# Kernel tuning notes

Hardware: AMD Instinct MI355X
Metric: run time of the kernel (lower is better)

Reference implementation:

```python
import jax, jax.numpy as jnp
import numpy as np

N = 100_000            # particles
E = 3_200_000          # edges (avg degree 32)
DIM = 3
H = 1.0                # kernel_radius
SIGMA = 3.0 / 359.0 / np.pi / H**3   # 3D quintic kernel normalization
RHO_REF = 1.0
P_REF = 100.0          # rho_ref * (10*u_ref)**2 / gamma, gamma=1
P_BG = 0.0             # p_bg_factor * p_ref
ETA0 = 0.01            # base_viscosity
EPS = 1e-8


def _qpows(d, p):
    q = d / H
    return (jnp.maximum(0.0, 1.0 - q) ** p,
            jnp.maximum(0.0, 2.0 - q) ** p,
            jnp.maximum(0.0, 3.0 - q) ** p)


def kernel_w(d):
    q1, q2, q3 = _qpows(d, 5)
    return SIGMA * (q3 - 6.0 * q2 + 15.0 * q1)


def kernel_grad_w(d):
    q1, q2, q3 = _qpows(d, 4)
    return (SIGMA / H) * (-5.0 * q3 + 30.0 * q2 - 75.0 * q1)


def setup_inputs() -> dict:
    key = jax.random.key(0)
    k1, k2, k3, k4 = jax.random.split(key, 4)
    r = jax.random.uniform(k1, (N, DIM), dtype=jnp.float32)   # positions in unit box
    v = jax.random.normal(k2, (N, DIM), dtype=jnp.float32)    # velocity history (last frame)
    i_s = jax.random.randint(k3, (E,), 0, N)                  # receivers
    j_s = jax.random.randint(k4, (E,), 0, N)                  # senders
    return {"r": r, "v": v, "i_s": i_s, "j_s": j_s}


def reference(r, v, i_s, j_s):
    n = r.shape[0]
    # --- per-edge gather + kernel ---
    dr = r[i_s] - r[j_s]                       # displacement_fn, [E,3]
    d = jnp.sqrt(jnp.sum(dr * dr, axis=-1))    # [E]
    w = kernel_w(d)
    # --- density summation (scatter) ---
    mass = jnp.ones((n,), r.dtype)
    rho = mass * jax.ops.segment_sum(w, i_s, num_segments=n)
    # Tait EoS, gamma=1
    p = P_REF * (rho / RHO_REF - 1.0) + P_BG
    eta = jnp.full((n,), ETA0, r.dtype)

    # --- per-edge acceleration (gather particle fields to edges) ---
    rho_i, rho_j = rho[i_s], rho[j_s]
    p_i, p_j = p[i_s], p[j_s]
    eta_i, eta_j = eta[i_s], eta[j_s]
    u_i, u_j = v[i_s], v[j_s]                  # u == v in _transform
    v_i, v_j = u_i, u_j

    eta_ij = 2.0 * eta_i * eta_j / (eta_i + eta_j + EPS)
    p_ij = (rho_j * p_i + rho_i * p_j) / (rho_i + rho_j)
    # ((m_i/rho_i)^2 + (m_j/rho_j)^2)/m_i with m == 1
    wvol = (1.0 / rho_i) ** 2 + (1.0 / rho_j) ** 2
    c = wvol * kernel_grad_w(d) / (d + EPS)    # [E]

    # transport stress A = (outer(rho_i*u_i, v_i-u_i) + outer(rho_j*u_j, v_j-u_j))/2, [E,3,3]
    A = 0.5 * (rho_i[:, None, None] * u_i[:, :, None] * (v_i - u_i)[:, None, :]
               + rho_j[:, None, None] * u_j[:, :, None] * (v_j - u_j)[:, None, :])
    Ar = jnp.einsum('eij,ej->ei', A, dr)

    a_eq_8 = c[:, None] * (-p_ij[:, None] * dr + Ar + eta_ij[:, None] * (u_i - u_j))
    p_bg_i = jnp.zeros_like(p_i)               # _transform passes zeros
    a_eq_13 = (c * p_bg_i)[:, None] * dr

    # --- scatter-reduce to particles ---
    dudt = jax.ops.segment_sum(a_eq_8, i_s, num_segments=n)   # [N,3]
    dvdt = jax.ops.segment_sum(a_eq_13, i_s, num_segments=n)  # [N,3]

    # pack state outputs: [rho, p, dudt(3), dvdt(3)] -> [N,8]
    return jnp.concatenate([rho[:, None], p[:, None], dudt, dvdt], axis=1)
```

## Files before the change

kernel.cpp:

```cpp
#include <hip/hip_runtime.h>
#include <math.h>

#ifndef M_PI
#define M_PI 3.14159265358979323846
#endif

static constexpr float kSigma = (float)(3.0 / 359.0 / M_PI);
static constexpr float kPRef  = 100.0f;
static constexpr float kEps   = 1e-8f;
static constexpr float kEta   = (float)(2.0 * 0.01 * 0.01 / (0.01 + 0.01 + 1e-8));

#define CHUNKA 8192

__device__ __forceinline__ float pow5f(float t) { float t2 = t * t; return t2 * t2 * t; }
__device__ __forceinline__ float pow4f(float t) { float t2 = t * t; return t2 * t2; }

__global__ void k_pack(const float* __restrict__ r, float4* __restrict__ pos4, int n) {
    int i = blockIdx.x * blockDim.x + threadIdx.x;
    if (i >= n) return;
    pos4[i] = make_float4(r[3 * i], r[3 * i + 1], r[3 * i + 2], 0.f);
}

__global__ void k_hist(const int* __restrict__ i_s, int* __restrict__ ghist,
                       int nbA, int nbins, int E, int shift) {
    __shared__ int h[512];
    int t = threadIdx.x, blk = blockIdx.x;
    for (int b = t; b < nbins; b += 512) h[b] = 0;
    __syncthreads();
    int base = blk * CHUNKA;
    int end = min(base + CHUNKA, E);
    for (int k = base + t; k < end; k += 512)
        atomicAdd(&h[i_s[k] >> shift], 1);
    __syncthreads();
    for (int b = t; b < nbins; b += 512)
        ghist[b * nbA + blk] = h[b];
}

__global__ void k_scan_block(const int* __restrict__ in, int* __restrict__ out,
                             int* __restrict__ bsum, int m) {
    __shared__ int s[256];
    int t = threadIdx.x;
    int i = blockIdx.x * 256 + t;
    int x = (i < m) ? in[i] : 0;
    s[t] = x;
    __syncthreads();
    for (int d = 1; d < 256; d <<= 1) {
        int v = (t >= d) ? s[t - d] : 0;
        __syncthreads();
        s[t] += v;
        __syncthreads();
    }
    if (i < m) out[i] = s[t] - x;
    if (t == 255) bsum[blockIdx.x] = s[255];
}

__global__ void k_scan_bsums(const int* __restrict__ bsum, int* __restrict__ bscan, int nb) {
    __shared__ int s[512];
    __shared__ int carry;
    int t = threadIdx.x;
    if (t == 0) carry = 0;
    __syncthreads();
    for (int base = 0; base < nb; base += 512) {
        int i = base + t;
        int x = (i < nb) ? bsum[i] : 0;
        s[t] = x;
        __syncthreads();
        for (int d = 1; d < 512; d <<= 1) {
            int v = (t >= d) ? s[t - d] : 0;
            __syncthreads();
            s[t] += v;
            __syncthreads();
        }
        if (i < nb) bscan[i] = s[t] - x + carry;
        __syncthreads();
        if (t == 511) carry += s[511];
        __syncthreads();
    }
}

__global__ void k_split(const int* __restrict__ i_s, const int* __restrict__ j_s,
                        const int* __restrict__ gscan, const int* __restrict__ bscan,
                        int* __restrict__ pairs, int nbA, int nbins, int E,
                        int shift, int jbits) {
    __shared__ int cur[512];
    int t = threadIdx.x, blk = blockIdx.x;
    for (int b = t; b < nbins; b += 512) {
        int idx = b * nbA + blk;
        cur[b] = gscan[idx] + bscan[idx >> 8];
    }
    __syncthreads();
    int fmask = (1 << shift) - 1;
    int base = blk * CHUNKA;
    int end = min(base + CHUNKA, E);
    for (int k = base + t; k < end; k += 512) {
        int i = i_s[k];
        int pos = atomicAdd(&cur[i >> shift], 1);
        pairs[pos] = ((i & fmask) << jbits) | j_s[k];
    }
}

__global__ void k_rho_bin(const float4* __restrict__ pos4, const float* __restrict__ v,
                          const int* __restrict__ pairs, const int* __restrict__ gscan,
                          const int* __restrict__ bscan, float4* __restrict__ pv8,
                          float* __restrict__ out, int nbA, int n, int E,
                          int shift, int jbits, int m) {
    __shared__ float srho[512];
    __shared__ float4 spos[512];
    __shared__ int sse[2];
    int b = blockIdx.x, t = threadIdx.x;
    int slots = 1 << shift;
    int lo = b << shift;
    for (int s0 = t; s0 < slots; s0 += 1024) {
        srho[s0] = 0.f;
        int i = lo + s0;
        spos[s0] = (i < n) ? pos4[i] : make_float4(0.f, 0.f, 0.f, 0.f);
    }
    if (t == 0) {
        int i0 = b * nbA;
        sse[0] = gscan[i0] + bscan[i0 >> 8];
        int i1 = (b + 1) * nbA;
        sse[1] = (i1 < m) ? (gscan[i1] + bscan[i1 >> 8]) : E;
    }
    __syncthreads();
    int s = sse[0], e = sse[1];
    int jm = (1 << jbits) - 1;
    for (int k = s + t; k < e; k += 1024) {
        int pr = pairs[k];
        int slot = pr >> jbits, j = pr & jm;
        float4 rj = pos4[j];
        float4 ri = spos[slot];
        float dx = ri.x - rj.x, dy = ri.y - rj.y, dz = ri.z - rj.z;
        float d = sqrtf(dx * dx + dy * dy + dz * dz);
        float t1 = fmaxf(1.f - d, 0.f);
        float t2 = fmaxf(2.f - d, 0.f);
        float t3 = fmaxf(3.f - d, 0.f);
        float w = kSigma * (pow5f(t3) - 6.f * pow5f(t2) + 15.f * pow5f(t1));
        atomicAdd(&srho[slot], w);
    }
    __syncthreads();
    for (int s0 = t; s0 < slots; s0 += 1024) {
        int i = lo + s0;
        if (i >= n) continue;
        float rh = srho[s0];
        float pp = kPRef * (rh - 1.0f);
        float4 sp = spos[s0];
        pv8[2 * i]     = make_float4(sp.x, sp.y, sp.z, rh);
        pv8[2 * i + 1] = make_float4(v[3 * i], v[3 * i + 1], v[3 * i + 2], pp);
        float* o = out + (size_t)i * 8;
        o[0] = rh;
        o[1] = pp;
        o[5] = 0.f; o[6] = 0.f; o[7] = 0.f;
    }
}

__global__ void k_acc_bin(const float4* __restrict__ pv8, const int* __restrict__ pairs,
                          const int* __restrict__ gscan, const int* __restrict__ bscan,
                          float* __restrict__ out, int nbA, int n, int E,
                          int shift, int jbits, int m) {
    __shared__ float sax[512], say[512], saz[512];
    __shared__ float4 sab[1024];
    __shared__ int sse[2];
    int b = blockIdx.x, t = threadIdx.x;
    int slots = 1 << shift;
    int lo = b << shift;
    for (int s0 = t; s0 < slots; s0 += 1024) { sax[s0] = 0.f; say[s0] = 0.f; saz[s0] = 0.f; }
    for (int q = t; q < 2 * slots; q += 1024) {
        int gi = 2 * lo + q;
        sab[q] = (gi < 2 * n) ? pv8[gi] : make_float4(0.f, 0.f, 0.f, 0.f);
    }
    if (t == 0) {
        int i0 = b * nbA;
        sse[0] = gscan[i0] + bscan[i0 >> 8];
        int i1 = (b + 1) * nbA;
        sse[1] = (i1 < m) ? (gscan[i1] + bscan[i1 >> 8]) : E;
    }
    __syncthreads();
    int s = sse[0], e = sse[1];
    int jm = (1 << jbits) - 1;
    for (int k = s + t; k < e; k += 1024) {
        int pr = pairs[k];
        int slot = pr >> jbits, j = pr & jm;
        float4 aj = pv8[2 * j];
        float4 bj = pv8[2 * j + 1];
        float4 ai = sab[2 * slot];
        float4 bi = sab[2 * slot + 1];
        float rho_i = ai.w, p_i = bi.w;
        float rho_j = aj.w, p_j = bj.w;
        float dx = ai.x - aj.x, dy = ai.y - aj.y, dz = ai.z - aj.z;
        float d = sqrtf(dx * dx + dy * dy + dz * dz);
        float t1 = fmaxf(1.f - d, 0.f);
        float t2 = fmaxf(2.f - d, 0.f);
        float t3 = fmaxf(3.f - d, 0.f);
        float gw = kSigma * (-5.f * pow4f(t3) + 30.f * pow4f(t2) - 75.f * pow4f(t1));
        float inv_i = 1.0f / rho_i, inv_j = 1.0f / rho_j;
        float c = (inv_i * inv_i + inv_j * inv_j) * gw / (d + kEps);
        float p_ij = (rho_j * p_i + rho_i * p_j) / (rho_i + rho_j);
        atomicAdd(&sax[slot], c * (kEta * (bi.x - bj.x) - p_ij * dx));
        atomicAdd(&say[slot], c * (kEta * (bi.y - bj.y) - p_ij * dy));
        atomicAdd(&saz[slot], c * (kEta * (bi.z - bj.z) - p_ij * dz));
    }
    __syncthreads();
    for (int s0 = t; s0 < slots; s0 += 1024) {
        int i = lo + s0;
        if (i >= n) continue;
        float* o = out + (size_t)i * 8 + 2;
        o[0] = sax[s0]; o[1] = say[s0]; o[2] = saz[s0];
    }
}

static inline char* wcarve(char*& ws, size_t bytes) {
    char* p = ws;
    ws += (bytes + 255) & ~(size_t)255;
    return p;
}

extern "C" void kernel_launch(void* const* d_in, const int* in_sizes, int n_in,
                              void* d_out, int out_size, void* d_ws, size_t ws_size,
                              hipStream_t stream) {
    const float* r = (const float*)d_in[0];
    const float* v = (const float*)d_in[1];
    const int* i_s = (const int*)d_in[2];
    const int* j_s = (const int*)d_in[3];
    int n = in_sizes[0] / 3;
    int E = in_sizes[2];
    float* out = (float*)d_out;

    int shift = 8;
    int nbins = ((n - 1) >> shift) + 1;
    while (nbins > 512) { shift++; nbins = ((n - 1) >> shift) + 1; }
    int jbits = 1;
    while ((1 << jbits) < n) jbits++;

    int nbA = (E + CHUNKA - 1) / CHUNKA;
    int m = nbins * nbA;
    int nb2 = (m + 255) / 256;

    char* ws = (char*)d_ws;
    float4* pos4  = (float4*)wcarve(ws, (size_t)n * 16);
    float4* pv8   = (float4*)wcarve(ws, (size_t)n * 32);
    int*    ghist = (int*)wcarve(ws, (size_t)m * 4);
    int*    gscan = (int*)wcarve(ws, (size_t)m * 4);
    int*    bsum  = (int*)wcarve(ws, (size_t)nb2 * 4);
    int*    bscan = (int*)wcarve(ws, (size_t)nb2 * 4);
    int*    pairs = (int*)wcarve(ws, (size_t)E * 4);

    const int bs = 256;
    int gn = (n + bs - 1) / bs;

    k_pack<<<gn, bs, 0, stream>>>(r, pos4, n);
    k_hist<<<nbA, 512, 0, stream>>>(i_s, ghist, nbA, nbins, E, shift);
    k_scan_block<<<nb2, 256, 0, stream>>>(ghist, gscan, bsum, m);
    k_scan_bsums<<<1, 512, 0, stream>>>(bsum, bscan, nb2);
    k_split<<<nbA, 512, 0, stream>>>(i_s, j_s, gscan, bscan, pairs, nbA, nbins, E, shift, jbits);
    k_rho_bin<<<nbins, 1024, 0, stream>>>(pos4, v, pairs, gscan, bscan, pv8, out, nbA, n, E, shift, jbits, m);
    k_acc_bin<<<nbins, 1024, 0, stream>>>(pv8, pairs, gscan, bscan, out, nbA, n, E, shift, jbits, m);
}
```

Measured before the change: 214.5 us.

## Split each bin's edges across eight sub-blocks with partial-sum reduction kernels

The per-bin density and acceleration kernels were one 1024-thread block per 256-particle bin (~391 blocks). Now each bin is split into eight sub-blocks of 256 threads, each handling a contiguous slice of the bin's edges. Each sub-block writes its shared-memory partial sums to global buffers, and new reduction kernels combine them and write the outputs. The histogram uses half-size chunks so the split kernel can index the finer scan at every other column. This raises block count and occupancy and cuts shared-atomic contention, at the cost of extra partial-buffer traffic and two extra launches.

Measured after the change: 210.9 us. No clear change (-1.6%).

```diff
diff --git a/kernel.cpp b/kernel.cpp
--- a/kernel.cpp
+++ b/kernel.cpp
@@ -10,7 +10,9 @@
 static constexpr float kEps   = 1e-8f;
 static constexpr float kEta   = (float)(2.0 * 0.01 * 0.01 / (0.01 + 0.01 + 1e-8));
 
-#define CHUNKA 8192
+#define CHUNKH 4096
+#define CHUNKS 8192
+#define NSUB   8
 
 __device__ __forceinline__ float pow5f(float t) { float t2 = t * t; return t2 * t2 * t; }
 __device__ __forceinline__ float pow4f(float t) { float t2 = t * t; return t2 * t2; }
@@ -22,18 +24,18 @@
 }
 
 __global__ void k_hist(const int* __restrict__ i_s, int* __restrict__ ghist,
-                       int nbA, int nbins, int E, int shift) {
+                       int nbAh, int nbins, int E, int shift) {
     __shared__ int h[512];
     int t = threadIdx.x, blk = blockIdx.x;
-    for (int b = t; b < nbins; b += 512) h[b] = 0;
-    __syncthreads();
-    int base = blk * CHUNKA;
-    int end = min(base + CHUNKA, E);
-    for (int k = base + t; k < end; k += 512)
+    for (int b = t; b < nbins; b += 256) h[b] = 0;
+    __syncthreads();
+    int base = blk * CHUNKH;
+    int end = min(base + CHUNKH, E);
+    for (int k = base + t; k < end; k += 256)
         atomicAdd(&h[i_s[k] >> shift], 1);
     __syncthreads();
-    for (int b = t; b < nbins; b += 512)
-        ghist[b * nbA + blk] = h[b];
+    for (int b = t; b < nbins; b += 256)
+        ghist[b * nbAh + blk] = h[b];
 }
 
 __global__ void k_scan_block(const int* __restrict__ in, int* __restrict__ out,
@@ -78,20 +80,23 @@
     }
 }
 
+__device__ __forceinline__ int scanned(const int* __restrict__ gscan,
+                                       const int* __restrict__ bscan, int idx) {
+    return gscan[idx] + bscan[idx >> 8];
+}
+
 __global__ void k_split(const int* __restrict__ i_s, const int* __restrict__ j_s,
                         const int* __restrict__ gscan, const int* __restrict__ bscan,
-                        int* __restrict__ pairs, int nbA, int nbins, int E,
+                        int* __restrict__ pairs, int nbAh, int nbins, int E,
                         int shift, int jbits) {
     __shared__ int cur[512];
     int t = threadIdx.x, blk = blockIdx.x;
-    for (int b = t; b < nbins; b += 512) {
-        int idx = b * nbA + blk;
-        cur[b] = gscan[idx] + bscan[idx >> 8];
-    }
+    for (int b = t; b < nbins; b += 512)
+        cur[b] = scanned(gscan, bscan, b * nbAh + 2 * blk);
     __syncthreads();
     int fmask = (1 << shift) - 1;
-    int base = blk * CHUNKA;
-    int end = min(base + CHUNKA, E);
+    int base = blk * CHUNKS;
+    int end = min(base + CHUNKS, E);
     for (int k = base + t; k < end; k += 512) {
         int i = i_s[k];
         int pos = atomicAdd(&cur[i >> shift], 1);
@@ -99,32 +104,29 @@
     }
 }
 
-__global__ void k_rho_bin(const float4* __restrict__ pos4, const float* __restrict__ v,
-                          const int* __restrict__ pairs, const int* __restrict__ gscan,
-                          const int* __restrict__ bscan, float4* __restrict__ pv8,
-                          float* __restrict__ out, int nbA, int n, int E,
-                          int shift, int jbits, int m) {
-    __shared__ float srho[512];
-    __shared__ float4 spos[512];
+__global__ void k_rho_bin(const float4* __restrict__ pos4, const int* __restrict__ pairs,
+                          const int* __restrict__ gscan, const int* __restrict__ bscan,
+                          float* __restrict__ part_rho, int nbAh, int n, int E,
+                          int shift, int jbits, int nbins) {
+    __shared__ float srho[256];
+    __shared__ float4 spos[256];
     __shared__ int sse[2];
-    int b = blockIdx.x, t = threadIdx.x;
-    int slots = 1 << shift;
-    int lo = b << shift;
-    for (int s0 = t; s0 < slots; s0 += 1024) {
-        srho[s0] = 0.f;
-        int i = lo + s0;
-        spos[s0] = (i < n) ? pos4[i] : make_float4(0.f, 0.f, 0.f, 0.f);
-    }
+    int bin = blockIdx.x >> 3, sub = blockIdx.x & (NSUB - 1);
+    int t = threadIdx.x;
+    int lo = bin << shift;
+    srho[t] = 0.f;
+    int ii = lo + t;
+    spos[t] = (ii < n) ? pos4[ii] : make_float4(0.f, 0.f, 0.f, 0.f);
     if (t == 0) {
-        int i0 = b * nbA;
-        sse[0] = gscan[i0] + bscan[i0 >> 8];
-        int i1 = (b + 1) * nbA;
-        sse[1] = (i1 < m) ? (gscan[i1] + bscan[i1 >> 8]) : E;
-    }
-    __syncthreads();
-    int s = sse[0], e = sse[1];
+        sse[0] = scanned(gscan, bscan, bin * nbAh);
+        sse[1] = (bin + 1 < nbins) ? scanned(gscan, bscan, (bin + 1) * nbAh) : E;
+    }
+    __syncthreads();
+    int s = sse[0], len = sse[1] - sse[0];
+    int k0 = s + (int)((long)len * sub / NSUB);
+    int k1 = s + (int)((long)len * (sub + 1) / NSUB);
     int jm = (1 << jbits) - 1;
-    for (int k = s + t; k < e; k += 1024) {
+    for (int k = k0 + t; k < k1; k += 256) {
         int pr = pairs[k];
         int slot = pr >> jbits, j = pr & jm;
         float4 rj = pos4[j];
@@ -138,46 +140,52 @@
         atomicAdd(&srho[slot], w);
     }
     __syncthreads();
-    for (int s0 = t; s0 < slots; s0 += 1024) {
-        int i = lo + s0;
-        if (i >= n) continue;
-        float rh = srho[s0];
-        float pp = kPRef * (rh - 1.0f);
-        float4 sp = spos[s0];
-        pv8[2 * i]     = make_float4(sp.x, sp.y, sp.z, rh);
-        pv8[2 * i + 1] = make_float4(v[3 * i], v[3 * i + 1], v[3 * i + 2], pp);
-        float* o = out + (size_t)i * 8;
-        o[0] = rh;
-        o[1] = pp;
-        o[5] = 0.f; o[6] = 0.f; o[7] = 0.f;
-    }
+    if (ii < n) part_rho[(size_t)sub * n + ii] = srho[t];
+}
+
+__global__ void k_reduce_rho(const float* __restrict__ part_rho,
+                             const float4* __restrict__ pos4, const float* __restrict__ v,
+                             float4* __restrict__ pv8, float* __restrict__ out, int n) {
+    int i = blockIdx.x * blockDim.x + threadIdx.x;
+    if (i >= n) return;
+    float rh = 0.f;
+    for (int s = 0; s < NSUB; s++) rh += part_rho[(size_t)s * n + i];
+    float pp = kPRef * (rh - 1.0f);
+    float4 sp = pos4[i];
+    pv8[2 * i]     = make_float4(sp.x, sp.y, sp.z, rh);
+    pv8[2 * i + 1] = make_float4(v[3 * i], v[3 * i + 1], v[3 * i + 2], pp);
+    float* o = out + (size_t)i * 8;
+    o[0] = rh;
+    o[1] = pp;
+    o[5] = 0.f; o[6] = 0.f; o[7] = 0.f;
 }
 
 __global__ void k_acc_bin(const float4* __restrict__ pv8, const int* __restrict__ pairs,
                           const int* __restrict__ gscan, const int* __restrict__ bscan,
-                          float* __restrict__ out, int nbA, int n, int E,
-                          int shift, int jbits, int m) {
-    __shared__ float sax[512], say[512], saz[512];
-    __shared__ float4 sab[1024];
+                          float* __restrict__ part_ax, float* __restrict__ part_ay,
+                          float* __restrict__ part_az, int nbAh, int n, int E,
+                          int shift, int jbits, int nbins) {
+    __shared__ float sax[256], say[256], saz[256];
+    __shared__ float4 sab[512];
     __shared__ int sse[2];
-    int b = blockIdx.x, t = threadIdx.x;
-    int slots = 1 << shift;
-    int lo = b << shift;
-    for (int s0 = t; s0 < slots; s0 += 1024) { sax[s0] = 0.f; say[s0] = 0.f; saz[s0] = 0.f; }
-    for (int q = t; q < 2 * slots; q += 1024) {
+    int bin = blockIdx.x >> 3, sub = blockIdx.x & (NSUB - 1);
+    int t = threadIdx.x;
+    int lo = bin << shift;
+    sax[t] = 0.f; say[t] = 0.f; saz[t] = 0.f;
+    for (int q = t; q < 512; q += 256) {
         int gi = 2 * lo + q;
-        sab[q] = (gi < 2 * n) ? pv8[gi] : make_float4(0.f, 0.f, 0.f, 0.f);
+        sab[q] = (gi < 2 * n) ? pv8[gi] : make_float4(1.f, 1.f, 1.f, 1.f);
     }
     if (t == 0) {
-        int i0 = b * nbA;
-        sse[0] = gscan[i0] + bscan[i0 >> 8];
-        int i1 = (b + 1) * nbA;
-        sse[1] = (i1 < m) ? (gscan[i1] + bscan[i1 >> 8]) : E;
-    }
-    __syncthreads();
-    int s = sse[0], e = sse[1];
+        sse[0] = scanned(gscan, bscan, bin * nbAh);
+        sse[1] = (bin + 1 < nbins) ? scanned(gscan, bscan, (bin + 1) * nbAh) : E;
+    }
+    __syncthreads();
+    int s = sse[0], len = sse[1] - sse[0];
+    int k0 = s + (int)((long)len * sub / NSUB);
+    int k1 = s + (int)((long)len * (sub + 1) / NSUB);
     int jm = (1 << jbits) - 1;
-    for (int k = s + t; k < e; k += 1024) {
+    for (int k = k0 + t; k < k1; k += 256) {
         int pr = pairs[k];
         int slot = pr >> jbits, j = pr & jm;
         float4 aj = pv8[2 * j];
@@ -200,12 +208,28 @@
         atomicAdd(&saz[slot], c * (kEta * (bi.z - bj.z) - p_ij * dz));
     }
     __syncthreads();
-    for (int s0 = t; s0 < slots; s0 += 1024) {
-        int i = lo + s0;
-        if (i >= n) continue;
-        float* o = out + (size_t)i * 8 + 2;
-        o[0] = sax[s0]; o[1] = say[s0]; o[2] = saz[s0];
-    }
+    int ii = lo + t;
+    if (ii < n) {
+        size_t o = (size_t)sub * n + ii;
+        part_ax[o] = sax[t];
+        part_ay[o] = say[t];
+        part_az[o] = saz[t];
+    }
+}
+
+__global__ void k_reduce_acc(const float* __restrict__ part_ax,
+                             const float* __restrict__ part_ay,
+                             const float* __restrict__ part_az,
+                             float* __restrict__ out, int n) {
+    int i = blockIdx.x * blockDim.x + threadIdx.x;
+    if (i >= n) return;
+    float ax = 0.f, ay = 0.f, az = 0.f;
+    for (int s = 0; s < NSUB; s++) {
+        size_t o = (size_t)s * n + i;
+        ax += part_ax[o]; ay += part_ay[o]; az += part_az[o];
+    }
+    float* o = out + (size_t)i * 8 + 2;
+    o[0] = ax; o[1] = ay; o[2] = az;
 }
 
 static inline char* wcarve(char*& ws, size_t bytes) {
@@ -231,27 +255,34 @@
     int jbits = 1;
     while ((1 << jbits) < n) jbits++;
 
-    int nbA = (E + CHUNKA - 1) / CHUNKA;
-    int m = nbins * nbA;
+    int nbAh = (E + CHUNKH - 1) / CHUNKH;
+    int nbAs = (E + CHUNKS - 1) / CHUNKS;
+    int m = nbins * nbAh;
     int nb2 = (m + 255) / 256;
 
     char* ws = (char*)d_ws;
-    float4* pos4  = (float4*)wcarve(ws, (size_t)n * 16);
-    float4* pv8   = (float4*)wcarve(ws, (size_t)n * 32);
-    int*    ghist = (int*)wcarve(ws, (size_t)m * 4);
-    int*    gscan = (int*)wcarve(ws, (size_t)m * 4);
-    int*    bsum  = (int*)wcarve(ws, (size_t)nb2 * 4);
-    int*    bscan = (int*)wcarve(ws, (size_t)nb2 * 4);
-    int*    pairs = (int*)wcarve(ws, (size_t)E * 4);
+    float4* pos4    = (float4*)wcarve(ws, (size_t)n * 16);
+    float4* pv8     = (float4*)wcarve(ws, (size_t)n * 32);
+    int*    ghist   = (int*)wcarve(ws, (size_t)m * 4);
+    int*    gscan   = (int*)wcarve(ws, (size_t)m * 4);
+    int*    bsum    = (int*)wcarve(ws, (size_t)nb2 * 4);
+    int*    bscan   = (int*)wcarve(ws, (size_t)nb2 * 4);
+    int*    pairs   = (int*)wcarve(ws, (size_t)E * 4);
+    float*  part_rho= (float*)wcarve(ws, (size_t)NSUB * n * 4);
+    float*  part_ax = (float*)wcarve(ws, (size_t)NSUB * n * 4);
+    float*  part_ay = (float*)wcarve(ws, (size_t)NSUB * n * 4);
+    float*  part_az = (float*)wcarve(ws, (size_t)NSUB * n * 4);
 
     const int bs = 256;
     int gn = (n + bs - 1) / bs;
 
     k_pack<<<gn, bs, 0, stream>>>(r, pos4, n);
-    k_hist<<<nbA, 512, 0, stream>>>(i_s, ghist, nbA, nbins, E, shift);
+    k_hist<<<nbAh, 256, 0, stream>>>(i_s, ghist, nbAh, nbins, E, shift);
     k_scan_block<<<nb2, 256, 0, stream>>>(ghist, gscan, bsum, m);
     k_scan_bsums<<<1, 512, 0, stream>>>(bsum, bscan, nb2);
-    k_split<<<nbA, 512, 0, stream>>>(i_s, j_s, gscan, bscan, pairs, nbA, nbins, E, shift, jbits);
-    k_rho_bin<<<nbins, 1024, 0, stream>>>(pos4, v, pairs, gscan, bscan, pv8, out, nbA, n, E, shift, jbits, m);
-    k_acc_bin<<<nbins, 1024, 0, stream>>>(pv8, pairs, gscan, bscan, out, nbA, n, E, shift, jbits, m);
-}
+    k_split<<<nbAs, 512, 0, stream>>>(i_s, j_s, gscan, bscan, pairs, nbAh, nbins, E, shift, jbits);
+    k_rho_bin<<<nbins * NSUB, 256, 0, stream>>>(pos4, pairs, gscan, bscan, part_rho, nbAh, n, E, shift, jbits, nbins);
+    k_reduce_rho<<<gn, bs, 0, stream>>>(part_rho, pos4, v, pv8, out, n);
+    k_acc_bin<<<nbins * NSUB, 256, 0, stream>>>(pv8, pairs, gscan, bscan, part_ax, part_ay, part_az, nbAh, n, E, shift, jbits, nbins);
+    k_reduce_acc<<<gn, bs, 0, stream>>>(part_ax, part_ay, part_az, out, n);
+}
```
